# Performance work log

Measured on AMD Instinct MI355X. Metric: run time of the kernel, lower is better.

The kernel has to match this reference:

```python
import jax, jax.numpy as jnp
import numpy as np

EMBED_DIM = 1024
NUM_HEADS = 16
HEAD_DIM = EMBED_DIM // NUM_HEADS
SCALE = HEAD_DIM ** -0.5


def setup_inputs() -> dict:
    key = jax.random.key(0)
    k_x, k_wqkv, k_bqkv, k_wp, k_bp = jax.random.split(key, 5)
    B, N = 2, 2048
    x = jax.random.normal(k_x, (B, N, EMBED_DIM), dtype=jnp.float32)
    # torch.nn.Linear default init: U(-1/sqrt(fan_in), 1/sqrt(fan_in))
    lim = 1.0 / np.sqrt(EMBED_DIM)
    W_qkv = jax.random.uniform(k_wqkv, (EMBED_DIM, 3 * EMBED_DIM), jnp.float32, -lim, lim)
    b_qkv = jax.random.uniform(k_bqkv, (3 * EMBED_DIM,), jnp.float32, -lim, lim)
    W_proj = jax.random.uniform(k_wp, (EMBED_DIM, EMBED_DIM), jnp.float32, -lim, lim)
    b_proj = jax.random.uniform(k_bp, (EMBED_DIM,), jnp.float32, -lim, lim)
    return {"x": x, "W_qkv": W_qkv, "b_qkv": b_qkv, "W_proj": W_proj, "b_proj": b_proj}


def reference(x, W_qkv, b_qkv, W_proj, b_proj):
    B, N, C = x.shape
    qkv = x @ W_qkv + b_qkv                              # [B, N, 3C]
    qkv = qkv.reshape(B, N, 3, NUM_HEADS, HEAD_DIM)
    qkv = jnp.transpose(qkv, (2, 0, 3, 1, 4))            # [3, B, H, N, D]
    q, k, v = qkv[0], qkv[1], qkv[2]
    attn = jnp.einsum('bhnd,bhmd->bhnm', q, k) * SCALE   # [B, H, N, N]
    attn = jax.nn.softmax(attn, axis=-1)
    out = jnp.einsum('bhnm,bhmd->bhnd', attn, v)         # [B, H, N, D]
    out = jnp.transpose(out, (0, 2, 1, 3)).reshape(B, N, C)
    return out @ W_proj + b_proj
```

## Files before the change

kernel.cpp:

```cpp
#include <hip/hip_runtime.h>
#include <math.h>

typedef unsigned short u16;
typedef _Float16 f16;
typedef f16 f16x8 __attribute__((ext_vector_type(8)));
typedef __fp16 hp16x2 __attribute__((ext_vector_type(2)));
typedef float f32x4 __attribute__((ext_vector_type(4)));

#define SEQ   2048
#define NH    16
#define HD    64
#define EMB   1024
#define NQKV  3072
#define BATCH 2
#define PSTR  72
#define QSCALE 0.18033688f

__device__ __forceinline__ u16 f2h(float f) {
  union { f16 h; u16 u; } w; w.h = (f16)f; return w.u;
}

__device__ __forceinline__ void gload16(const void* g, void* l) {
  __builtin_amdgcn_global_load_lds(
      (const __attribute__((address_space(1))) unsigned int*)g,
      (__attribute__((address_space(3))) unsigned int*)l, 16, 0, 0);
}

__global__ __launch_bounds__(256) void cvt_x(const float* __restrict__ X,
                                             u16* __restrict__ Xh) {
  const size_t i = ((size_t)blockIdx.x * 256 + threadIdx.x) * 8;
  float4 a = *reinterpret_cast<const float4*>(&X[i]);
  float4 b = *reinterpret_cast<const float4*>(&X[i + 4]);
  union { hp16x2 h2[4]; float4 f; } pk;
  pk.h2[0] = __builtin_amdgcn_cvt_pkrtz(a.x, a.y);
  pk.h2[1] = __builtin_amdgcn_cvt_pkrtz(a.z, a.w);
  pk.h2[2] = __builtin_amdgcn_cvt_pkrtz(b.x, b.y);
  pk.h2[3] = __builtin_amdgcn_cvt_pkrtz(b.z, b.w);
  *reinterpret_cast<float4*>(&Xh[i]) = pk.f;
}

__global__ __launch_bounds__(256) void cvt_wt(const float* __restrict__ W,
                                              u16* __restrict__ Wt,
                                              int K, int N) {
  __shared__ u16 T[64][68];
  const int n0 = blockIdx.x << 6, k0 = blockIdx.y << 6;
  const int t = threadIdx.x;
  const int rr = t >> 4, cc = (t & 15) << 2;
#pragma unroll
  for (int p = 0; p < 4; p++) {
    const int kr = p * 16 + rr;
    float4 v = *reinterpret_cast<const float4*>(&W[(size_t)(k0 + kr) * N + n0 + cc]);
    T[cc + 0][kr] = f2h(v.x); T[cc + 1][kr] = f2h(v.y);
    T[cc + 2][kr] = f2h(v.z); T[cc + 3][kr] = f2h(v.w);
  }
  __syncthreads();
#pragma unroll
  for (int p = 0; p < 4; p++) {
    const int nr = p * 16 + rr;
    union { u16 s[4]; unsigned long long d; } o;
    o.s[0] = T[nr][cc + 0]; o.s[1] = T[nr][cc + 1];
    o.s[2] = T[nr][cc + 2]; o.s[3] = T[nr][cc + 3];
    *reinterpret_cast<unsigned long long*>(&Wt[(size_t)(n0 + nr) * K + k0 + cc]) = o.d;
  }
}

__device__ __forceinline__ void gemm_core(const u16* __restrict__ Ag,
                                          const u16* __restrict__ Bg,
                                          int m0, int n0, int t,
                                          f32x4 acc[4][4]) {
  __shared__ __align__(16) u16 As[128 * 32];
  __shared__ __align__(16) u16 Bs[128 * 32];
  const int lane = t & 63, w = t >> 6;
  const int l15  = lane & 15, quad = lane >> 4;
  const int wm = w >> 1, wn = w & 1;
  const int srow  = lane >> 2;
  const int gslot = (lane & 3) ^ ((srow >> 1) & 3);
  const int xk    = (quad ^ ((l15 >> 1) & 3)) << 3;

  for (int k0 = 0; k0 < EMB; k0 += 32) {
    __syncthreads();
#pragma unroll
    for (int i = 0; i < 2; i++) {
      const int ca = w * 2 + i;
      const int arow = ca * 16 + srow;
      gload16(Ag + (size_t)(m0 + arow) * EMB + k0 + gslot * 8, &As[ca * 512]);
      gload16(Bg + (size_t)(n0 + arow) * EMB + k0 + gslot * 8, &Bs[ca * 512]);
    }
    __syncthreads();
    f16x8 af[4], bf[4];
#pragma unroll
    for (int s = 0; s < 4; s++)
      af[s] = *reinterpret_cast<const f16x8*>(&As[(wm * 64 + s * 16 + l15) * 32 + xk]);
#pragma unroll
    for (int s = 0; s < 4; s++)
      bf[s] = *reinterpret_cast<const f16x8*>(&Bs[(wn * 64 + s * 16 + l15) * 32 + xk]);
#pragma unroll
    for (int i = 0; i < 4; i++)
#pragma unroll
      for (int j = 0; j < 4; j++)
        acc[i][j] = __builtin_amdgcn_mfma_f32_16x16x32_f16(af[i], bf[j], acc[i][j], 0, 0, 0);
  }
}

__global__ __launch_bounds__(256) void k_qkv(const u16* __restrict__ Ag,
                                             const u16* __restrict__ Bg,
                                             const float* __restrict__ bias,
                                             u16* __restrict__ qo,
                                             u16* __restrict__ ko,
                                             u16* __restrict__ vo) {
  const int t = threadIdx.x;
  const int lane = t & 63, w = t >> 6;
  const int l15 = lane & 15, quad = lane >> 4;
  const int wm = w >> 1, wn = w & 1;
  const int m0 = blockIdx.y << 7, n0 = blockIdx.x << 7;
  f32x4 acc[4][4];
#pragma unroll
  for (int i = 0; i < 4; i++)
#pragma unroll
    for (int j = 0; j < 4; j++) acc[i][j] = (f32x4){0.f, 0.f, 0.f, 0.f};
  gemm_core(Ag, Bg, m0, n0, t, acc);
#pragma unroll
  for (int j = 0; j < 4; j++) {
    const int c = n0 + wn * 64 + j * 16 + l15;
    const int which = c >> 10, h = (c >> 6) & 15, d = c & 63;
    const float bv = bias[c];
    const float sc = (which == 0) ? QSCALE : 1.0f;
#pragma unroll
    for (int i = 0; i < 4; i++) {
#pragma unroll
      for (int r = 0; r < 4; r++) {
        const int m  = m0 + wm * 64 + i * 16 + quad * 4 + r;
        const int bb = m >> 11, n = m & (SEQ - 1);
        const u16 val = f2h((acc[i][j][r] + bv) * sc);
        if (which == 2)
          vo[(((size_t)bb * NH + h) * HD + d) * SEQ + n] = val;
        else if (which == 1)
          ko[((((size_t)bb * NH + h) * SEQ) + n) * HD + d] = val;
        else
          qo[((((size_t)bb * NH + h) * SEQ) + n) * HD + d] = val;
      }
    }
  }
}

__global__ __launch_bounds__(256) void k_proj(const u16* __restrict__ Ag,
                                              const u16* __restrict__ Bg,
                                              const float* __restrict__ bias,
                                              float* __restrict__ out) {
  const int t = threadIdx.x;
  const int lane = t & 63, w = t >> 6;
  const int l15 = lane & 15, quad = lane >> 4;
  const int wm = w >> 1, wn = w & 1;
  const int m0 = blockIdx.y << 7, n0 = blockIdx.x << 7;
  f32x4 acc[4][4];
#pragma unroll
  for (int i = 0; i < 4; i++)
#pragma unroll
    for (int j = 0; j < 4; j++) acc[i][j] = (f32x4){0.f, 0.f, 0.f, 0.f};
  gemm_core(Ag, Bg, m0, n0, t, acc);
#pragma unroll
  for (int j = 0; j < 4; j++) {
    const int c = n0 + wn * 64 + j * 16 + l15;
    const float bv = bias[c];
#pragma unroll
    for (int i = 0; i < 4; i++) {
#pragma unroll
      for (int r = 0; r < 4; r++) {
        const int m = m0 + wm * 64 + i * 16 + quad * 4 + r;
        out[(size_t)m * EMB + c] = acc[i][j][r] + bv;
      }
    }
  }
}

__global__ __launch_bounds__(256) void k_attn(const u16* __restrict__ Qg,
                                              const u16* __restrict__ Kg,
                                              const u16* __restrict__ Vtg,
                                              u16* __restrict__ AO) {
  __shared__ __align__(16) u16 Ks[64 * 64];
  __shared__ __align__(16) u16 Vs[64 * 64];
  __shared__ __align__(16) u16 Ps[4 * 16 * PSTR];
  const int t    = threadIdx.x;
  const int lane = t & 63, w = t >> 6;
  const int l15  = lane & 15, quad = lane >> 4;
  const int bh   = blockIdx.y;
  const int q0   = blockIdx.x << 6;
  const size_t base = (size_t)bh * SEQ * HD;

  f16x8 qf[2];
  {
    const u16* qp = Qg + base + (size_t)(q0 + 16 * w + l15) * HD + quad * 8;
    union { float4 f; f16x8 v; } fu;
    fu.f = *reinterpret_cast<const float4*>(qp);        qf[0] = fu.v;
    fu.f = *reinterpret_cast<const float4*>(qp + 32);   qf[1] = fu.v;
  }

  f32x4 O4[4];
#pragma unroll
  for (int s = 0; s < 4; s++) O4[s] = (f32x4){0.f, 0.f, 0.f, 0.f};
  float lsum = 0.f;

  const int srw = lane >> 3;
  const int ssl = lane & 7;
  u16* Pw = &Ps[w * 16 * PSTR];

  for (int kt = 0; kt < SEQ; kt += 64) {
    __syncthreads();
#pragma unroll
    for (int i = 0; i < 2; i++) {
      const int ca  = w * 2 + i;
      const int row = ca * 8 + srw;
      const int sg  = (ssl ^ ((row >> 1) & 7)) << 3;
      gload16(Kg  + base + (size_t)(kt + row) * HD + sg, &Ks[ca * 512]);
      gload16(Vtg + base + (size_t)row * SEQ + kt + sg,  &Vs[ca * 512]);
    }
    __syncthreads();

    float sv[4][4];
#pragma unroll
    for (int s = 0; s < 4; s++) {
      const int row = s * 16 + l15;
      const int f   = (row >> 1) & 7;
      f16x8 kf0 = *reinterpret_cast<const f16x8*>(&Ks[row * 64 + ((quad ^ f) << 3)]);
      f16x8 kf1 = *reinterpret_cast<const f16x8*>(&Ks[row * 64 + (((4 + quad) ^ f) << 3)]);
      f32x4 c = (f32x4){0.f, 0.f, 0.f, 0.f};
      c = __builtin_amdgcn_mfma_f32_16x16x32_f16(kf0, qf[0], c, 0, 0, 0);
      c = __builtin_amdgcn_mfma_f32_16x16x32_f16(kf1, qf[1], c, 0, 0, 0);
#pragma unroll
      for (int r = 0; r < 4; r++) {
        const float p = exp2f(c[r]);
        sv[s][r] = p;
        lsum += p;
      }
    }

#pragma unroll
    for (int s = 0; s < 4; s++) {
      union { hp16x2 h2[2]; unsigned long long d; } pk;
      pk.h2[0] = __builtin_amdgcn_cvt_pkrtz(sv[s][0], sv[s][1]);
      pk.h2[1] = __builtin_amdgcn_cvt_pkrtz(sv[s][2], sv[s][3]);
      *reinterpret_cast<unsigned long long*>(&Pw[l15 * PSTR + s * 16 + quad * 4]) = pk.d;
    }
    f16x8 pf0 = *reinterpret_cast<const f16x8*>(&Pw[l15 * PSTR + quad * 8]);
    f16x8 pf1 = *reinterpret_cast<const f16x8*>(&Pw[l15 * PSTR + 32 + quad * 8]);

#pragma unroll
    for (int s = 0; s < 4; s++) {
      const int row = s * 16 + l15;
      const int f   = (row >> 1) & 7;
      f16x8 vf0 = *reinterpret_cast<const f16x8*>(&Vs[row * 64 + ((quad ^ f) << 3)]);
      f16x8 vf1 = *reinterpret_cast<const f16x8*>(&Vs[row * 64 + (((4 + quad) ^ f) << 3)]);
      O4[s] = __builtin_amdgcn_mfma_f32_16x16x32_f16(pf0, vf0, O4[s], 0, 0, 0);
      O4[s] = __builtin_amdgcn_mfma_f32_16x16x32_f16(pf1, vf1, O4[s], 0, 0, 0);
    }
  }

  lsum += __shfl_xor(lsum, 16);
  lsum += __shfl_xor(lsum, 32);
  const int b = bh >> 4, h = bh & 15;
#pragma unroll
  for (int r = 0; r < 4; r++) {
    const float inv = 1.f / __shfl(lsum, quad * 4 + r, 64);
    const int n = q0 + 16 * w + quad * 4 + r;
    u16* dst = AO + ((size_t)(b * SEQ + n)) * EMB + h * HD;
#pragma unroll
    for (int s = 0; s < 4; s++) dst[s * 16 + l15] = f2h(O4[s][r] * inv);
  }
}

extern "C" void kernel_launch(void* const* d_in, const int* in_sizes, int n_in,
                              void* d_out, int out_size, void* d_ws, size_t ws_size,
                              hipStream_t stream) {
  (void)in_sizes; (void)n_in; (void)out_size; (void)ws_size;
  const float* x     = (const float*)d_in[0];
  const float* Wqkv  = (const float*)d_in[1];
  const float* bqkv  = (const float*)d_in[2];
  const float* Wproj = (const float*)d_in[3];
  const float* bproj = (const float*)d_in[4];
  float* out = (float*)d_out;

  const size_t NE = (size_t)BATCH * SEQ * EMB;
  u16* q    = (u16*)d_ws;
  u16* k    = q + NE;
  u16* vt   = k + NE;
  u16* aoxh = vt + NE;
  u16* Wt   = aoxh + NE;
  u16* Wpt  = Wt + (size_t)NQKV * EMB;

  cvt_x<<<NE / 2048, 256, 0, stream>>>(x, aoxh);
  dim3 gw1(NQKV / 64, EMB / 64);
  cvt_wt<<<gw1, 256, 0, stream>>>(Wqkv, Wt, EMB, NQKV);
  dim3 gw2(EMB / 64, EMB / 64);
  cvt_wt<<<gw2, 256, 0, stream>>>(Wproj, Wpt, EMB, EMB);

  dim3 gq(NQKV / 128, (BATCH * SEQ) / 128);
  k_qkv<<<gq, 256, 0, stream>>>(aoxh, Wt, bqkv, q, k, vt);

  dim3 ga(SEQ / 64, BATCH * NH);
  k_attn<<<ga, 256, 0, stream>>>(q, k, vt, aoxh);

  dim3 gp(EMB / 128, (BATCH * SEQ) / 128);
  k_proj<<<gp, 256, 0, stream>>>(aoxh, Wpt, bproj, out);
}
```

Before: 218.4 us.

## Switch attention kernel to 32x32x16 MFMA with 128-query blocks

```diff
diff --git a/kernel.cpp b/kernel.cpp
--- a/kernel.cpp
+++ b/kernel.cpp
@@ -6,6 +6,7 @@
 typedef f16 f16x8 __attribute__((ext_vector_type(8)));
 typedef __fp16 hp16x2 __attribute__((ext_vector_type(2)));
 typedef float f32x4 __attribute__((ext_vector_type(4)));
+typedef float f32x16 __attribute__((ext_vector_type(16)));
 
 #define SEQ   2048
 #define NH    16
@@ -179,30 +180,30 @@
                                               u16* __restrict__ AO) {
   __shared__ __align__(16) u16 Ks[64 * 64];
   __shared__ __align__(16) u16 Vs[64 * 64];
-  __shared__ __align__(16) u16 Ps[4 * 16 * PSTR];
+  __shared__ __align__(16) u16 Ps[4 * 32 * PSTR];
   const int t    = threadIdx.x;
   const int lane = t & 63, w = t >> 6;
-  const int l15  = lane & 15, quad = lane >> 4;
+  const int l31  = lane & 31, hi = lane >> 5;
   const int bh   = blockIdx.y;
-  const int q0   = blockIdx.x << 6;
+  const int q0   = blockIdx.x << 7;
   const size_t base = (size_t)bh * SEQ * HD;
 
-  f16x8 qf[2];
+  f16x8 qf[4];
   {
-    const u16* qp = Qg + base + (size_t)(q0 + 16 * w + l15) * HD + quad * 8;
-    union { float4 f; f16x8 v; } fu;
-    fu.f = *reinterpret_cast<const float4*>(qp);        qf[0] = fu.v;
-    fu.f = *reinterpret_cast<const float4*>(qp + 32);   qf[1] = fu.v;
-  }
-
-  f32x4 O4[4];
-#pragma unroll
-  for (int s = 0; s < 4; s++) O4[s] = (f32x4){0.f, 0.f, 0.f, 0.f};
+    const u16* qp = Qg + base + (size_t)(q0 + 32 * w + l31) * HD + hi * 8;
+#pragma unroll
+    for (int c = 0; c < 4; c++) {
+      union { float4 f; f16x8 v; } fu;
+      fu.f = *reinterpret_cast<const float4*>(qp + c * 16);
+      qf[c] = fu.v;
+    }
+  }
+
+  f32x16 O0 = {}, O1 = {};
   float lsum = 0.f;
-
-  const int srw = lane >> 3;
-  const int ssl = lane & 7;
-  u16* Pw = &Ps[w * 16 * PSTR];
+  const int fsw = (l31 >> 1) & 7;
+  const int srw = lane >> 3, ssl = lane & 7;
+  u16* Pw = &Ps[w * 32 * PSTR];
 
   for (int kt = 0; kt < SEQ; kt += 64) {
     __syncthreads();
@@ -216,55 +217,56 @@
     }
     __syncthreads();
 
-    float sv[4][4];
-#pragma unroll
-    for (int s = 0; s < 4; s++) {
-      const int row = s * 16 + l15;
-      const int f   = (row >> 1) & 7;
-      f16x8 kf0 = *reinterpret_cast<const f16x8*>(&Ks[row * 64 + ((quad ^ f) << 3)]);
-      f16x8 kf1 = *reinterpret_cast<const f16x8*>(&Ks[row * 64 + (((4 + quad) ^ f) << 3)]);
-      f32x4 c = (f32x4){0.f, 0.f, 0.f, 0.f};
-      c = __builtin_amdgcn_mfma_f32_16x16x32_f16(kf0, qf[0], c, 0, 0, 0);
-      c = __builtin_amdgcn_mfma_f32_16x16x32_f16(kf1, qf[1], c, 0, 0, 0);
-#pragma unroll
-      for (int r = 0; r < 4; r++) {
-        const float p = exp2f(c[r]);
-        sv[s][r] = p;
-        lsum += p;
+#pragma unroll
+    for (int sk = 0; sk < 2; sk++) {
+      f32x16 c = {};
+#pragma unroll
+      for (int cc = 0; cc < 4; cc++) {
+        f16x8 kf = *reinterpret_cast<const f16x8*>(
+            &Ks[(sk * 32 + l31) * 64 + (((cc * 2 + hi) ^ fsw) << 3)]);
+        c = __builtin_amdgcn_mfma_f32_32x32x16_f16(kf, qf[cc], c, 0, 0, 0);
       }
-    }
-
-#pragma unroll
-    for (int s = 0; s < 4; s++) {
-      union { hp16x2 h2[2]; unsigned long long d; } pk;
-      pk.h2[0] = __builtin_amdgcn_cvt_pkrtz(sv[s][0], sv[s][1]);
-      pk.h2[1] = __builtin_amdgcn_cvt_pkrtz(sv[s][2], sv[s][3]);
-      *reinterpret_cast<unsigned long long*>(&Pw[l15 * PSTR + s * 16 + quad * 4]) = pk.d;
-    }
-    f16x8 pf0 = *reinterpret_cast<const f16x8*>(&Pw[l15 * PSTR + quad * 8]);
-    f16x8 pf1 = *reinterpret_cast<const f16x8*>(&Pw[l15 * PSTR + 32 + quad * 8]);
-
-#pragma unroll
-    for (int s = 0; s < 4; s++) {
-      const int row = s * 16 + l15;
-      const int f   = (row >> 1) & 7;
-      f16x8 vf0 = *reinterpret_cast<const f16x8*>(&Vs[row * 64 + ((quad ^ f) << 3)]);
-      f16x8 vf1 = *reinterpret_cast<const f16x8*>(&Vs[row * 64 + (((4 + quad) ^ f) << 3)]);
-      O4[s] = __builtin_amdgcn_mfma_f32_16x16x32_f16(pf0, vf0, O4[s], 0, 0, 0);
-      O4[s] = __builtin_amdgcn_mfma_f32_16x16x32_f16(pf1, vf1, O4[s], 0, 0, 0);
-    }
-  }
-
-  lsum += __shfl_xor(lsum, 16);
+#pragma unroll
+      for (int g = 0; g < 4; g++) {
+        const float p0 = exp2f(c[4 * g + 0]);
+        const float p1 = exp2f(c[4 * g + 1]);
+        const float p2 = exp2f(c[4 * g + 2]);
+        const float p3 = exp2f(c[4 * g + 3]);
+        lsum += (p0 + p1) + (p2 + p3);
+        union { hp16x2 h2[2]; unsigned long long d; } pk;
+        pk.h2[0] = __builtin_amdgcn_cvt_pkrtz(p0, p1);
+        pk.h2[1] = __builtin_amdgcn_cvt_pkrtz(p2, p3);
+        *reinterpret_cast<unsigned long long*>(
+            &Pw[l31 * PSTR + sk * 32 + g * 8 + 4 * hi]) = pk.d;
+      }
+    }
+
+#pragma unroll
+    for (int cc = 0; cc < 4; cc++) {
+      f16x8 pf = *reinterpret_cast<const f16x8*>(&Pw[l31 * PSTR + cc * 16 + hi * 8]);
+      f16x8 vf0 = *reinterpret_cast<const f16x8*>(
+          &Vs[l31 * 64 + (((cc * 2 + hi) ^ fsw) << 3)]);
+      f16x8 vf1 = *reinterpret_cast<const f16x8*>(
+          &Vs[(32 + l31) * 64 + (((cc * 2 + hi) ^ fsw) << 3)]);
+      O0 = __builtin_amdgcn_mfma_f32_32x32x16_f16(pf, vf0, O0, 0, 0, 0);
+      O1 = __builtin_amdgcn_mfma_f32_32x32x16_f16(pf, vf1, O1, 0, 0, 0);
+    }
+  }
+
   lsum += __shfl_xor(lsum, 32);
   const int b = bh >> 4, h = bh & 15;
 #pragma unroll
-  for (int r = 0; r < 4; r++) {
-    const float inv = 1.f / __shfl(lsum, quad * 4 + r, 64);
-    const int n = q0 + 16 * w + quad * 4 + r;
-    u16* dst = AO + ((size_t)(b * SEQ + n)) * EMB + h * HD;
-#pragma unroll
-    for (int s = 0; s < 4; s++) dst[s * 16 + l15] = f2h(O4[s][r] * inv);
+  for (int g = 0; g < 4; g++) {
+#pragma unroll
+    for (int rr = 0; rr < 4; rr++) {
+      const int r = g * 4 + rr;
+      const int qrow = rr + 8 * g + 4 * hi;
+      const float inv = 1.f / __shfl(lsum, qrow, 64);
+      const int n = q0 + 32 * w + qrow;
+      u16* dst = AO + ((size_t)(b * SEQ + n)) * EMB + h * HD;
+      dst[l31]      = f2h(O0[r] * inv);
+      dst[32 + l31] = f2h(O1[r] * inv);
+    }
   }
 }
 
@@ -296,7 +298,7 @@
   dim3 gq(NQKV / 128, (BATCH * SEQ) / 128);
   k_qkv<<<gq, 256, 0, stream>>>(aoxh, Wt, bqkv, q, k, vt);
 
-  dim3 ga(SEQ / 64, BATCH * NH);
+  dim3 ga(SEQ / 128, BATCH * NH);
   k_attn<<<ga, 256, 0, stream>>>(q, k, vt, aoxh);
 
   dim3 gp(EMB / 128, (BATCH * SEQ) / 128);
```

Result: no change. 218.2 us (-0.1%).
